# Kernel tuning notes

Hardware: AMD Instinct MI355X
Metric: run time of the kernel (lower is better)

The kernel has to match this reference:

```python
import jax, jax.numpy as jnp
import numpy as np

TEMPERATURE = 0.5


def setup_inputs() -> dict:
    key = jax.random.key(0)
    ks = jax.random.split(key, 12)
    B, N, T = 128, 64, 256
    IN, H, OUT = N + T, 256, 128
    E = N * (N - 1) // 2  # 2016 upper-tri edges per graph
    total_edges = B * E
    inp = {
        "x_topology": jax.random.normal(ks[0], (B, N, N), jnp.float32),
        "x_temporal": jax.random.normal(ks[1], (B, N, T), jnp.float32),
        "gumbel_u": jax.random.uniform(ks[2], (total_edges,), jnp.float32, 1e-6, 1.0),
        # GNNLayer linear
        "W_gnn": jax.random.normal(ks[3], (IN, H), jnp.float32) / np.sqrt(IN),
        "b_gnn": jnp.zeros((H,), jnp.float32),
        # edge heads (input dim 2*H)
        "W_mean": jax.random.normal(ks[4], (2 * H, OUT), jnp.float32) / np.sqrt(2 * H),
        "b_mean": jnp.zeros((OUT,), jnp.float32),
        "W_var": jax.random.normal(ks[5], (2 * H, OUT), jnp.float32) / np.sqrt(2 * H),
        "b_var": jnp.zeros((OUT,), jnp.float32),
        "W_w": jax.random.normal(ks[6], (2 * H, 1), jnp.float32) / np.sqrt(2 * H),
        "b_w": jnp.zeros((1,), jnp.float32),
    }
    return inp


def reference(x_topology, x_temporal, gumbel_u, W_gnn, b_gnn,
              W_mean, b_mean, W_var, b_var, W_w, b_w):
    B, N, _ = x_topology.shape
    T = x_temporal.shape[-1]
    # Upper-triangular fully-connected edge index (no self loops), batched with node offsets.
    row, col = jnp.triu_indices(N, k=1)          # [E]
    E = row.shape[0]
    offs = (jnp.arange(B) * N)[:, None]          # [B,1]
    src = (row[None, :] + offs).reshape(-1)       # [B*E]
    dst = (col[None, :] + offs).reshape(-1)       # [B*E]

    # Node features: concat topology + temporal, flatten batch of graphs.
    x = jnp.concatenate([x_topology, x_temporal], axis=-1).reshape(B * N, N + T)

    # Mean aggregation (PyG aggr='mean'): messages x[src] scattered to dst; 0 for isolated nodes.
    msg_sum = jax.ops.segment_sum(x[src], dst, num_segments=B * N)      # [B*N, N+T]
    cnt = jax.ops.segment_sum(jnp.ones_like(src, x.dtype), dst, num_segments=B * N)
    agg = jnp.where(cnt[:, None] > 0, msg_sum / jnp.maximum(cnt, 1.0)[:, None], 0.0)

    h = jax.nn.relu(agg @ W_gnn + b_gnn)          # [B*N, H]

    # Edge MLP heads on gathered [src||dst] embeddings.
    ef = jnp.concatenate([h[src], h[dst]], axis=-1)        # [B*E, 2H]
    mean = ef @ W_mean + b_mean                             # [B*E, OUT]
    variance = jax.nn.softplus(ef @ W_var + b_var) + 1e-6   # [B*E, OUT]
    weight = jax.nn.sigmoid((ef @ W_w + b_w)[:, 0])          # [B*E]

    # Gumbel-softmax over the flattened edge-weight vector (dim=-1 of a 1-D tensor).
    g = -jnp.log(-jnp.log(gumbel_u))
    gumbel_w = jax.nn.softmax((weight + g) / TEMPERATURE, axis=-1)

    # Gaussian similarity per edge, scatter into dense adjacency.
    sim = jnp.exp(-0.5 * jnp.mean(mean ** 2 / (variance + 1e-8), axis=-1))
    edge_w = sim * gumbel_w                                  # [B*E]

    b_idx = jnp.repeat(jnp.arange(B), E)
    adj = jnp.zeros((B, N, N), x.dtype).at[b_idx, jnp.tile(row, B), jnp.tile(col, B)].set(edge_w)
    return adj
```

## Files before the change

### kernel.cpp

```cpp
#include <hip/hip_runtime.h>
#include <hip/hip_bf16.h>
#include <math.h>

#define Bg   128
#define Nn   64
#define Tt   256
#define INF  320
#define Hd   256
#define OUTD 128
#define Ee   2016
#define TOTE (Bg*Ee)
#define SCOLS 576
#define MROWS 8192

#define RSQRT_LN2 1.2011224087864498f
#define LOG2E     1.4426950408889634f
#define EPS_T     1.45719e-6f

typedef __attribute__((ext_vector_type(8))) short bf16x8;
typedef __attribute__((ext_vector_type(4))) float f32x4;

static __device__ __forceinline__ ushort f2bf(float v) {
    __hip_bfloat16 h = __float2bfloat16(v);
    return *(ushort*)&h;
}

#define CVT_N (INF * Hd)
#define PACK_N (Hd * SCOLS)
__global__ void k_prep(const float* __restrict__ Wg, const float* __restrict__ Wm,
                       const float* __restrict__ Wv, const float* __restrict__ Ww,
                       const float* __restrict__ bm, const float* __restrict__ bv,
                       const float* __restrict__ bw,
                       ushort* __restrict__ WgbT, ushort* __restrict__ WcatT,
                       float* __restrict__ ebias, unsigned* __restrict__ red) {
    int idx = blockIdx.x * 256 + threadIdx.x;
    if (idx == 0) { red[0] = 0u; red[1] = 0u; }
    if (idx < CVT_N) {
        int n = idx / INF, k = idx - n * INF;
        WgbT[idx] = f2bf(Wg[k * Hd + n]);
        return;
    }
    idx -= CVT_N;
    if (idx < PACK_N) {
        int n = idx / Hd, k = idx - n * Hd;
        float v = 0.f;
        if (n < 128)       v = Wm[k * 128 + n];
        else if (n < 256)  v = Wm[(256 + k) * 128 + (n - 128)];
        else if (n < 384)  v = Wv[k * 128 + (n - 256)];
        else if (n < 512)  v = Wv[(256 + k) * 128 + (n - 384)];
        else if (n == 512) v = Ww[k];
        else if (n == 513) v = Ww[256 + k];
        WcatT[idx] = f2bf(v);
        return;
    }
    idx -= PACK_N;
    if (idx >= SCOLS) return;
    float e = 0.f;
    if (idx < 128)                    e = bm[idx];
    else if (idx >= 256 && idx < 384) e = bv[idx - 256];
    else if (idx == 512)              e = bw[0];
    ebias[idx] = e;
}

__global__ __launch_bounds__(256) void k_agg(const float* __restrict__ topo,
                                             const float* __restrict__ temp,
                                             ushort* __restrict__ agg) {
    __shared__ float T[64 * 65];
    const int b = blockIdx.x, ft = blockIdx.y;
    const int tid = threadIdx.x;
    const int row = tid >> 2, seg = tid & 3;
    const float* src = (ft == 0) ? (topo + (size_t)(b * Nn + row) * Nn)
                                 : (temp + (size_t)(b * Nn + row) * Tt + (ft - 1) * 64);
    #pragma unroll
    for (int i = 0; i < 4; ++i) {
        float4 v = *(const float4*)(src + seg * 16 + i * 4);
        float* d = &T[row * 65 + seg * 16 + i * 4];
        d[0] = v.x; d[1] = v.y; d[2] = v.z; d[3] = v.w;
    }
    __syncthreads();
    const int w = tid >> 6, lane = tid & 63;
    #pragma unroll
    for (int k = 0; k < 16; ++k) {
        int f = w * 16 + k;
        float x = T[lane * 65 + f];
        float incl = x;
        #pragma unroll
        for (int o = 1; o < 64; o <<= 1) {
            float t = __shfl_up(incl, o);
            if (lane >= o) incl += t;
        }
        float excl = incl - x;
        T[lane * 65 + f] = lane ? excl * __builtin_amdgcn_rcpf((float)lane) : 0.f;
    }
    __syncthreads();
    const int node = tid >> 2, f0 = (tid & 3) * 16;
    ushort tmp[16];
    #pragma unroll
    for (int i = 0; i < 16; ++i) tmp[i] = f2bf(T[node * 65 + f0 + i]);
    ushort* dst = agg + (size_t)(b * Nn + node) * INF + ft * 64 + f0;
    *(uint4*)dst = *(uint4*)tmp;
    *(uint4*)(dst + 8) = *(uint4*)(tmp + 8);
}

__global__ __launch_bounds__(256) void k_gemm_mfma(const ushort* __restrict__ A,
                                                   const ushort* __restrict__ BT,
                                                   const float* __restrict__ bias,
                                                   ushort* __restrict__ Cb,
                                                   float* __restrict__ Cf,
                                                   int N, int K, int relu, int transC,
                                                   int edgeScale) {
    __shared__ ushort Asl[64 * 72];
    __shared__ ushort Bsl[64 * 72];
    const int tid = threadIdx.x;
    const int w = tid >> 6, lane = tid & 63;
    const int quad = lane >> 4, r16 = lane & 15;
    const int m0 = blockIdx.y * 64, n0 = blockIdx.x * 64;
    const int row = tid >> 2, seg = tid & 3;
    f32x4 acc[4] = {};

    for (int k0 = 0; k0 < K; k0 += 64) {
        const ushort* ap = A + (size_t)(m0 + row) * K + k0 + seg * 16;
        uint4 a0 = ((const uint4*)ap)[0];
        uint4 a1 = ((const uint4*)ap)[1];
        *(uint4*)(Asl + row * 72 + seg * 16)     = a0;
        *(uint4*)(Asl + row * 72 + seg * 16 + 8) = a1;
        const ushort* bp = BT + (size_t)(n0 + row) * K + k0 + seg * 16;
        uint4 b0 = ((const uint4*)bp)[0];
        uint4 b1 = ((const uint4*)bp)[1];
        *(uint4*)(Bsl + row * 72 + seg * 16)     = b0;
        *(uint4*)(Bsl + row * 72 + seg * 16 + 8) = b1;
        __syncthreads();

        bf16x8 af0 = *(const bf16x8*)(Asl + (w * 16 + r16) * 72 + quad * 8);
        bf16x8 af1 = *(const bf16x8*)(Asl + (w * 16 + r16) * 72 + 32 + quad * 8);
        #pragma unroll
        for (int ns = 0; ns < 4; ++ns) {
            bf16x8 bf0 = *(const bf16x8*)(Bsl + (ns * 16 + r16) * 72 + quad * 8);
            bf16x8 bf1 = *(const bf16x8*)(Bsl + (ns * 16 + r16) * 72 + 32 + quad * 8);
            acc[ns] = __builtin_amdgcn_mfma_f32_16x16x32_bf16(af0, bf0, acc[ns], 0, 0, 0);
            acc[ns] = __builtin_amdgcn_mfma_f32_16x16x32_bf16(af1, bf1, acc[ns], 0, 0, 0);
        }
        __syncthreads();
    }

    const int row0 = m0 + w * 16 + quad * 4;
    #pragma unroll
    for (int ns = 0; ns < 4; ++ns) {
        f32x4 a = acc[ns];
        int col = n0 + ns * 16 + r16;
        float bb = bias ? bias[col] : 0.f;
        float vv[4];
        #pragma unroll
        for (int i = 0; i < 4; ++i) {
            float v = a[i] + bb;
            if (relu) v = fmaxf(v, 0.f);
            vv[i] = v;
        }
        if (transC) {
            if (edgeScale) {
                if (col < 256) {
                    #pragma unroll
                    for (int i = 0; i < 4; ++i) vv[i] *= RSQRT_LN2;
                } else if (col < 512) {
                    #pragma unroll
                    for (int i = 0; i < 4; ++i)
                        vv[i] = __builtin_amdgcn_exp2f(vv[i] * LOG2E);
                }
            }
            *(float4*)(Cf + (size_t)col * MROWS + row0) = make_float4(vv[0], vv[1], vv[2], vv[3]);
        } else {
            #pragma unroll
            for (int i = 0; i < 4; ++i) {
                int row2 = row0 + i;
                if (Cb) Cb[(size_t)row2 * N + col] = f2bf(vv[i]);
                else    Cf[(size_t)row2 * N + col] = vv[i];
            }
        }
    }
}

static __device__ __forceinline__ float et(float mA, float mB, float eA, float eB) {
    float m = mA + mB;
    float E = eA * eB;
    float t = __builtin_amdgcn_logf(1.f + E) + EPS_T;
    return m * m * __builtin_amdgcn_rcpf(t);
}

__global__ __launch_bounds__(256, 4) void k_edge4(const float* __restrict__ ST,
                                                  const float* __restrict__ gu,
                                                  float* __restrict__ numer,
                                                  unsigned* __restrict__ red) {
    __shared__ float L[4][16][68];
    __shared__ float sred[4];
    const int bid = blockIdx.x;
    const int xcd = bid & 7, k = bid >> 3;
    const int b = xcd * 16 + k / 10;
    const int p = k - (k / 10) * 10;
    const int G0v[10] = {0,0,0,0,1,1,1,2,2,3};
    const int G1v[10] = {0,1,2,3,1,2,3,2,3,3};
    const int g0 = G0v[p], g1 = G1v[p];
    const int tid = threadIdx.x;

    int i, j;
    bool valid;
    if (g0 != g1) {
        i = tid >> 4; j = tid & 15; valid = true;
    } else {
        valid = tid < 120;
        int ii = 0, rr = tid;
        if (valid) { while (rr >= 15 - ii) { rr -= 15 - ii; ++ii; } }
        i = valid ? ii : 0;
        j = valid ? (ii + 1 + rr) : 1;
    }

    const int c = tid >> 2, nq = tid & 3;
    float acc = 0.f;
    #pragma unroll
    for (int h = 0; h < 2; ++h) {
        if (h) __syncthreads();
        #pragma unroll
        for (int arr = 0; arr < 4; ++arr) {
            const int g = (arr & 1) ? g1 : g0;
            float4 v = *(const float4*)&ST[(size_t)((arr << 7) + (h << 6) + c) * MROWS
                                           + b * 64 + (g << 4) + (nq << 2)];
            L[arr][nq * 4 + 0][c] = v.x;
            L[arr][nq * 4 + 1][c] = v.y;
            L[arr][nq * 4 + 2][c] = v.z;
            L[arr][nq * 4 + 3][c] = v.w;
        }
        __syncthreads();
        if (valid) {
            #pragma unroll 4
            for (int t = 0; t < 64; t += 4) {
                float4 mi = *(const float4*)&L[0][i][t];
                float4 mj = *(const float4*)&L[1][j][t];
                float4 ei = *(const float4*)&L[2][i][t];
                float4 ej = *(const float4*)&L[3][j][t];
                acc += et(mi.x, mj.x, ei.x, ej.x);
                acc += et(mi.y, mj.y, ei.y, ej.y);
                acc += et(mi.z, mj.z, ei.z, ej.z);
                acc += et(mi.w, mj.w, ei.w, ej.w);
            }
        }
    }

    const int ni = g0 * 16 + i, nj = g1 * 16 + j;
    float en = 0.f;
    if (valid) {
        int e = b * Ee + (ni * (127 - ni)) / 2 + (nj - ni - 1);
        float se = __expf(acc * (-1.f / 256.f));
        float wr = ST[(size_t)512 * MROWS + b * 64 + ni]
                 + ST[(size_t)513 * MROWS + b * 64 + nj];
        float w  = __builtin_amdgcn_rcpf(1.f + __expf(-wr));
        float g  = -__logf(-__logf(gu[e]));
        en = __expf((w + g) * 2.0f);
        numer[e] = se * en;
    }
    #pragma unroll
    for (int o = 32; o; o >>= 1) en += __shfl_down(en, o);
    if ((tid & 63) == 0) sred[tid >> 6] = en;
    __syncthreads();
    if (tid == 0) atomicAdd((float*)&red[1], sred[0] + sred[1] + sred[2] + sred[3]);
}

__global__ void k_out(const float* __restrict__ numer, const unsigned* __restrict__ red,
                      float* __restrict__ out) {
    int idx = blockIdx.x * 256 + threadIdx.x;
    if (idx >= Bg * Nn * Nn) return;
    int b = idx >> 12;
    int rem = idx & 4095;
    int r = rem >> 6, c = rem & 63;
    float v = 0.f;
    if (c > r) {
        int e = b * Ee + (r * (127 - r)) / 2 + (c - r - 1);
        float Sinv = __builtin_amdgcn_rcpf(((const float*)red)[1]);
        v = numer[e] * Sinv;
    }
    out[idx] = v;
}

extern "C" void kernel_launch(void* const* d_in, const int* in_sizes, int n_in,
                              void* d_out, int out_size, void* d_ws, size_t ws_size,
                              hipStream_t stream) {
    const float* topo = (const float*)d_in[0];
    const float* temp = (const float*)d_in[1];
    const float* gu   = (const float*)d_in[2];
    const float* Wg   = (const float*)d_in[3];
    const float* bg   = (const float*)d_in[4];
    const float* Wm   = (const float*)d_in[5];
    const float* bm   = (const float*)d_in[6];
    const float* Wv   = (const float*)d_in[7];
    const float* bv   = (const float*)d_in[8];
    const float* Ww   = (const float*)d_in[9];
    const float* bw   = (const float*)d_in[10];
    float* out = (float*)d_out;

    char* ws = (char*)d_ws;
    size_t off = 0;
    auto carve = [&](size_t bytes) { char* p = ws + off; off = (off + bytes + 255) & ~(size_t)255; return p; };

    char*   r1    = carve((size_t)SCOLS * MROWS * 4);
    float*  ST    = (float*)r1;
    ushort* aggb  = (ushort*)r1;
    ushort* hb    = (ushort*)carve((size_t)MROWS * Hd * 2);
    ushort* WgbT  = (ushort*)carve((size_t)INF * Hd * 2);
    ushort* WcatT = (ushort*)carve((size_t)Hd * SCOLS * 2);
    float*  ebias = (float*)carve((size_t)SCOLS * 4);
    float*  numer = (float*)carve((size_t)TOTE * 4);
    unsigned* red = (unsigned*)carve(256);

    k_prep<<<(CVT_N + PACK_N + SCOLS + 255) / 256, 256, 0, stream>>>(
        Wg, Wm, Wv, Ww, bm, bv, bw, WgbT, WcatT, ebias, red);
    k_agg<<<dim3(Bg, INF / 64), 256, 0, stream>>>(topo, temp, aggb);
    k_gemm_mfma<<<dim3(Hd / 64, MROWS / 64), 256, 0, stream>>>(
        aggb, WgbT, bg, hb, nullptr, Hd, INF, 1, 0, 0);
    k_gemm_mfma<<<dim3(SCOLS / 64, MROWS / 64), 256, 0, stream>>>(
        hb, WcatT, ebias, nullptr, ST, SCOLS, Hd, 0, 1, 1);
    k_edge4<<<Bg * 10, 256, 0, stream>>>(ST, gu, numer, red);
    k_out<<<(Bg * Nn * Nn + 255) / 256, 256, 0, stream>>>(numer, red, out);
}
```

Before: 133.5 us.

## Register-block edge kernel 2x2 per thread, split channels across waves, prefetch second half

Restructures the per-edge Gaussian-similarity kernel so each thread computes a 2x2 block of node pairs over a 16-channel slice, with the four waves covering different channel slices and combining partial sums through shared memory. This reuses each LDS load across two pairs and balances work in diagonal tiles, where previously half the threads sat idle. The second channel half is now prefetched from global memory into registers while the first half is computed. The cost is extra register pressure, an added cross-wave reduction step and more barriers.

Measured after the change: 132.1 us. About the same (-1.1%).

```diff
diff --git a/kernel.cpp b/kernel.cpp
--- a/kernel.cpp
+++ b/kernel.cpp
@@ -186,79 +186,117 @@
     return m * m * __builtin_amdgcn_rcpf(t);
 }
 
+static __device__ __forceinline__ float et4(float4 ma, float4 mb, float4 ea, float4 eb) {
+    return et(ma.x, mb.x, ea.x, eb.x) + et(ma.y, mb.y, ea.y, eb.y)
+         + et(ma.z, mb.z, ea.z, eb.z) + et(ma.w, mb.w, ea.w, eb.w);
+}
+
+static __device__ __forceinline__ void cphase(const float (*L)[16][68], int w,
+                                              int i0, int i1, int j0, int j1,
+                                              float& a00, float& a01,
+                                              float& a10, float& a11) {
+    #pragma unroll 2
+    for (int s = 0; s < 4; ++s) {
+        const int t = (w << 4) + (s << 2);
+        float4 mi0 = *(const float4*)&L[0][i0][t];
+        float4 mi1 = *(const float4*)&L[0][i1][t];
+        float4 mj0 = *(const float4*)&L[1][j0][t];
+        float4 mj1 = *(const float4*)&L[1][j1][t];
+        float4 ei0 = *(const float4*)&L[2][i0][t];
+        float4 ei1 = *(const float4*)&L[2][i1][t];
+        float4 ej0 = *(const float4*)&L[3][j0][t];
+        float4 ej1 = *(const float4*)&L[3][j1][t];
+        a00 += et4(mi0, mj0, ei0, ej0);
+        a01 += et4(mi0, mj1, ei0, ej1);
+        a10 += et4(mi1, mj0, ei1, ej0);
+        a11 += et4(mi1, mj1, ei1, ej1);
+    }
+}
+
 __global__ __launch_bounds__(256, 4) void k_edge4(const float* __restrict__ ST,
                                                   const float* __restrict__ gu,
                                                   float* __restrict__ numer,
                                                   unsigned* __restrict__ red) {
     __shared__ float L[4][16][68];
     __shared__ float sred[4];
+    float* R = &L[0][0][0];
     const int bid = blockIdx.x;
-    const int xcd = bid & 7, k = bid >> 3;
-    const int b = xcd * 16 + k / 10;
-    const int p = k - (k / 10) * 10;
+    const int xcd = bid & 7, kb = bid >> 3;
+    const int b = xcd * 16 + kb / 10;
+    const int p = kb - (kb / 10) * 10;
     const int G0v[10] = {0,0,0,0,1,1,1,2,2,3};
     const int G1v[10] = {0,1,2,3,1,2,3,2,3,3};
     const int g0 = G0v[p], g1 = G1v[p];
     const int tid = threadIdx.x;
-
-    int i, j;
-    bool valid;
-    if (g0 != g1) {
-        i = tid >> 4; j = tid & 15; valid = true;
-    } else {
-        valid = tid < 120;
-        int ii = 0, rr = tid;
-        if (valid) { while (rr >= 15 - ii) { rr -= 15 - ii; ++ii; } }
-        i = valid ? ii : 0;
-        j = valid ? (ii + 1 + rr) : 1;
-    }
+    const int w = tid >> 6, lane = tid & 63;
+
+    const int ci = lane >> 3, cj = lane & 7;
+    const int i0 = ci * 2, i1 = ci * 2 + 1;
+    const int j0 = cj * 2, j1 = cj * 2 + 1;
+    const bool cvalid = (g0 != g1) || (ci <= cj);
 
     const int c = tid >> 2, nq = tid & 3;
-    float acc = 0.f;
-    #pragma unroll
-    for (int h = 0; h < 2; ++h) {
-        if (h) __syncthreads();
-        #pragma unroll
-        for (int arr = 0; arr < 4; ++arr) {
-            const int g = (arr & 1) ? g1 : g0;
-            float4 v = *(const float4*)&ST[(size_t)((arr << 7) + (h << 6) + c) * MROWS
-                                           + b * 64 + (g << 4) + (nq << 2)];
-            L[arr][nq * 4 + 0][c] = v.x;
-            L[arr][nq * 4 + 1][c] = v.y;
-            L[arr][nq * 4 + 2][c] = v.z;
-            L[arr][nq * 4 + 3][c] = v.w;
-        }
-        __syncthreads();
-        if (valid) {
-            #pragma unroll 4
-            for (int t = 0; t < 64; t += 4) {
-                float4 mi = *(const float4*)&L[0][i][t];
-                float4 mj = *(const float4*)&L[1][j][t];
-                float4 ei = *(const float4*)&L[2][i][t];
-                float4 ej = *(const float4*)&L[3][j][t];
-                acc += et(mi.x, mj.x, ei.x, ej.x);
-                acc += et(mi.y, mj.y, ei.y, ej.y);
-                acc += et(mi.z, mj.z, ei.z, ej.z);
-                acc += et(mi.w, mj.w, ei.w, ej.w);
-            }
-        }
-    }
-
-    const int ni = g0 * 16 + i, nj = g1 * 16 + j;
+    const size_t cbase = (size_t)b * 64;
+
+    #pragma unroll
+    for (int arr = 0; arr < 4; ++arr) {
+        const int g = (arr & 1) ? g1 : g0;
+        float4 v = *(const float4*)&ST[(size_t)((arr << 7) + c) * MROWS
+                                       + cbase + (g << 4) + (nq << 2)];
+        L[arr][nq * 4 + 0][c] = v.x;
+        L[arr][nq * 4 + 1][c] = v.y;
+        L[arr][nq * 4 + 2][c] = v.z;
+        L[arr][nq * 4 + 3][c] = v.w;
+    }
+    __syncthreads();
+
+    float4 p1[4];
+    #pragma unroll
+    for (int arr = 0; arr < 4; ++arr) {
+        const int g = (arr & 1) ? g1 : g0;
+        p1[arr] = *(const float4*)&ST[(size_t)((arr << 7) + 64 + c) * MROWS
+                                      + cbase + (g << 4) + (nq << 2)];
+    }
+
+    float a00 = 0.f, a01 = 0.f, a10 = 0.f, a11 = 0.f;
+    if (cvalid) cphase(L, w, i0, i1, j0, j1, a00, a01, a10, a11);
+    __syncthreads();
+
+    #pragma unroll
+    for (int arr = 0; arr < 4; ++arr) {
+        L[arr][nq * 4 + 0][c] = p1[arr].x;
+        L[arr][nq * 4 + 1][c] = p1[arr].y;
+        L[arr][nq * 4 + 2][c] = p1[arr].z;
+        L[arr][nq * 4 + 3][c] = p1[arr].w;
+    }
+    __syncthreads();
+    if (cvalid) cphase(L, w, i0, i1, j0, j1, a00, a01, a10, a11);
+    __syncthreads();
+
+    *(float4*)&R[(w << 8) + (lane << 2)] = make_float4(a00, a01, a10, a11);
+    __syncthreads();
+
+    const int cell = tid >> 2, k = tid & 3;
+    const int tci = cell >> 3, tcj = cell & 7;
+    const int ti = 2 * tci + (k >> 1), tj = 2 * tcj + (k & 1);
+    const int ni = g0 * 16 + ti, nj = g1 * 16 + tj;
+    const bool tvalid = (g0 != g1) || (ti < tj);
     float en = 0.f;
-    if (valid) {
+    if (tvalid) {
+        float a = R[tid] + R[256 + tid] + R[512 + tid] + R[768 + tid];
         int e = b * Ee + (ni * (127 - ni)) / 2 + (nj - ni - 1);
-        float se = __expf(acc * (-1.f / 256.f));
-        float wr = ST[(size_t)512 * MROWS + b * 64 + ni]
-                 + ST[(size_t)513 * MROWS + b * 64 + nj];
-        float w  = __builtin_amdgcn_rcpf(1.f + __expf(-wr));
-        float g  = -__logf(-__logf(gu[e]));
-        en = __expf((w + g) * 2.0f);
+        float se = __expf(a * (-1.f / 256.f));
+        float wr = ST[(size_t)512 * MROWS + cbase + ni]
+                 + ST[(size_t)513 * MROWS + cbase + nj];
+        float wgt = __builtin_amdgcn_rcpf(1.f + __expf(-wr));
+        float g   = -__logf(-__logf(gu[e]));
+        en = __expf((wgt + g) * 2.0f);
         numer[e] = se * en;
     }
-    #pragma unroll
-    for (int o = 32; o; o >>= 1) en += __shfl_down(en, o);
-    if ((tid & 63) == 0) sred[tid >> 6] = en;
+    float s = en;
+    #pragma unroll
+    for (int o = 32; o; o >>= 1) s += __shfl_down(s, o);
+    if ((tid & 63) == 0) sred[tid >> 6] = s;
     __syncthreads();
     if (tid == 0) atomicAdd((float*)&red[1], sred[0] + sred[1] + sred[2] + sred[3]);
 }
```
